# Kernel optimization log

Hardware: AMD Instinct MI355X
Metric: run time of the kernel (lower is better)

## Reference

```python
import jax, jax.numpy as jnp
import numpy as np

K_NEIGH = 20
THRES = 0.5


def setup_inputs() -> dict:
    key = jax.random.key(0)
    # pairwise distance matrix: (batch, num_points, num_points)
    x = jax.random.uniform(key, (16, 4096, 4096), dtype=jnp.float32)
    return {"x": x}


def reference(x):
    # top_k over negated distances == k smallest distances
    vals, nn_idx = jax.lax.top_k(-x, K_NEIGH)          # (B, N, k)
    n = x.shape[1]
    # self index per row, broadcast over k (matches to_add tile in TF code)
    self_idx = jnp.broadcast_to(
        jnp.arange(n, dtype=nn_idx.dtype)[:, None], (n, K_NEIGH)
    )                                                   # (N, k)
    # where distance > thres (i.e. vals < -thres), replace neighbor with self
    mask = vals < -THRES                                # (B, N, k) bool
    nn_idx = jnp.where(mask, self_idx[None, :, :], nn_idx)
    return jax.lax.stop_gradient(nn_idx)
```

## Files before the change

### kernel.cpp

```cpp
#include <hip/hip_runtime.h>
#include <stdint.h>

#define K_NEIGH 20
#define THRES   0.5f
#define NPTS    4096
#define BLOCK   256
#define CAP     256

__global__ __launch_bounds__(BLOCK)
void knn_topk_kernel(const float* __restrict__ x, int* __restrict__ out) {
    const int row  = blockIdx.x;
    const int self = row & (NPTS - 1);
    const int tid  = threadIdx.x;
    const float* __restrict__ xr = x + (size_t)row * NPTS;

    float v[16];
#pragma unroll
    for (int m = 0; m < 4; ++m) {
        float4 f = ((const float4*)xr)[tid + 256 * m];
        v[4*m+0] = f.x; v[4*m+1] = f.y; v[4*m+2] = f.z; v[4*m+3] = f.w;
    }

    __shared__ unsigned long long keys[CAP];
    __shared__ int cnt;
    __shared__ unsigned long long warpmin[4];

    if (tid == 0) cnt = 0;
    __syncthreads();

    const float T = 0.02f;
    int local = 0;
#pragma unroll
    for (int e = 0; e < 16; ++e) local += (v[e] < T) ? 1 : 0;

    int base = 0;
    if (local) base = atomicAdd(&cnt, local);
    if (local && base + local <= CAP) {
        int o = base;
#pragma unroll
        for (int m = 0; m < 4; ++m) {
#pragma unroll
            for (int j = 0; j < 4; ++j) {
                float val = v[4*m + j];
                if (val < T) {
                    unsigned idx = 4u*tid + 1024u*m + j;
                    keys[o++] = ((unsigned long long)__float_as_uint(val) << 32) | idx;
                }
            }
        }
    }
    __syncthreads();
    const int total = cnt;

    if (total >= K_NEIGH && total <= CAP) {
        if (tid >= total) keys[tid] = ~0ULL;
        __syncthreads();
        for (int k = 2; k <= CAP; k <<= 1) {
            for (int j = k >> 1; j > 0; j >>= 1) {
                int ixj = tid ^ j;
                if (ixj > tid) {
                    unsigned long long a = keys[tid];
                    unsigned long long b = keys[ixj];
                    bool up = ((tid & k) == 0);
                    if ((a > b) == up) { keys[tid] = b; keys[ixj] = a; }
                }
                __syncthreads();
            }
        }
        if (tid < K_NEIGH) {
            unsigned long long kk = keys[tid];
            float val = __uint_as_float((unsigned)(kk >> 32));
            int   idx = (int)(kk & 0xFFFFFFFFu);
            out[(size_t)row * K_NEIGH + tid] = (val > THRES) ? self : idx;
        }
    } else {
        for (int sel = 0; sel < K_NEIGH; ++sel) {
            unsigned long long best = ~0ULL;
#pragma unroll
            for (int m = 0; m < 4; ++m) {
#pragma unroll
                for (int j = 0; j < 4; ++j) {
                    unsigned long long kk =
                        ((unsigned long long)__float_as_uint(v[4*m + j]) << 32) |
                        (4u*tid + 1024u*m + j);
                    if (kk < best) best = kk;
                }
            }
            for (int off = 32; off; off >>= 1) {
                unsigned long long o = __shfl_down(best, off);
                if (o < best) best = o;
            }
            if ((tid & 63) == 0) warpmin[tid >> 6] = best;
            __syncthreads();
            if (tid == 0) {
                unsigned long long b0 = warpmin[0];
                for (int w = 1; w < 4; ++w) if (warpmin[w] < b0) b0 = warpmin[w];
                warpmin[0] = b0;
            }
            __syncthreads();
            unsigned long long win = warpmin[0];
            if (tid == 0) {
                float val = __uint_as_float((unsigned)(win >> 32));
                int   idx = (int)(win & 0xFFFFFFFFu);
                out[(size_t)row * K_NEIGH + sel] = (val > THRES) ? self : idx;
            }
            unsigned widx  = (unsigned)(win & 0xFFFFFFFFu);
            int      owner = (int)((widx >> 2) & 255u);
            if (tid == owner) v[4*(widx >> 10) + (widx & 3u)] = __uint_as_float(0x7F800000u);
            __syncthreads();
        }
    }
}

extern "C" void kernel_launch(void* const* d_in, const int* in_sizes, int n_in,
                              void* d_out, int out_size, void* d_ws, size_t ws_size,
                              hipStream_t stream) {
    const float* x  = (const float*)d_in[0];
    int*        out = (int*)d_out;
    const int n_rows = in_sizes[0] / NPTS;
    knn_topk_kernel<<<n_rows, BLOCK, 0, stream>>>(x, out);
}
```

Measured before the change: 1.427 ms.

## Process one row per wavefront and replace bitonic sort with shuffle selection

Each 64-lane wavefront now handles a whole row instead of a 256-thread block per row, so a block covers four rows and no block-level barriers are needed. The candidate keys are selected with 20 rounds of wave-wide shuffle-min over four registers per lane, replacing the shared-memory bitonic sort. The fallback path uses a strictly-increasing-key selection instead of owner invalidation. Each lane now holds 64 floats, which raises register pressure and may limit occupancy despite the launch bound hint. The shared atomic counter per wave is read without a barrier, relying on wave-synchronous execution.

```diff
diff --git a/kernel.cpp b/kernel.cpp
--- a/kernel.cpp
+++ b/kernel.cpp
@@ -4,111 +4,106 @@
 #define K_NEIGH 20
 #define THRES   0.5f
 #define NPTS    4096
-#define BLOCK   256
+#define WAVES   4
+#define BLOCK   (64 * WAVES)
 #define CAP     256
+#define TCAND   0.02f
 
-__global__ __launch_bounds__(BLOCK)
-void knn_topk_kernel(const float* __restrict__ x, int* __restrict__ out) {
-    const int row  = blockIdx.x;
+__global__ __launch_bounds__(BLOCK, 4)
+void knn_topk_wave(const float* __restrict__ x, int* __restrict__ out) {
+    const int wave = threadIdx.x >> 6;
+    const int lane = threadIdx.x & 63;
+    const int row  = blockIdx.x * WAVES + wave;
     const int self = row & (NPTS - 1);
-    const int tid  = threadIdx.x;
     const float* __restrict__ xr = x + (size_t)row * NPTS;
 
-    float v[16];
+    __shared__ unsigned long long keys[WAVES][CAP];
+    __shared__ int cnt[WAVES];
+
+    if (lane == 0) cnt[wave] = 0;
+
+    float4 f[16];
 #pragma unroll
-    for (int m = 0; m < 4; ++m) {
-        float4 f = ((const float4*)xr)[tid + 256 * m];
-        v[4*m+0] = f.x; v[4*m+1] = f.y; v[4*m+2] = f.z; v[4*m+3] = f.w;
+    for (int m = 0; m < 16; ++m) f[m] = ((const float4*)xr)[lane + 64 * m];
+
+    int local = 0;
+#pragma unroll
+    for (int m = 0; m < 16; ++m) {
+        local += (f[m].x < TCAND) + (f[m].y < TCAND) +
+                 (f[m].z < TCAND) + (f[m].w < TCAND);
     }
 
-    __shared__ unsigned long long keys[CAP];
-    __shared__ int cnt;
-    __shared__ unsigned long long warpmin[4];
-
-    if (tid == 0) cnt = 0;
-    __syncthreads();
-
-    const float T = 0.02f;
-    int local = 0;
-#pragma unroll
-    for (int e = 0; e < 16; ++e) local += (v[e] < T) ? 1 : 0;
-
     int base = 0;
-    if (local) base = atomicAdd(&cnt, local);
+    if (local) base = atomicAdd(&cnt[wave], local);
     if (local && base + local <= CAP) {
         int o = base;
 #pragma unroll
-        for (int m = 0; m < 4; ++m) {
+        for (int m = 0; m < 16; ++m) {
+            const unsigned eb = 4u * ((unsigned)lane + 64u * m);
+            const float vv[4] = { f[m].x, f[m].y, f[m].z, f[m].w };
 #pragma unroll
             for (int j = 0; j < 4; ++j) {
-                float val = v[4*m + j];
-                if (val < T) {
-                    unsigned idx = 4u*tid + 1024u*m + j;
-                    keys[o++] = ((unsigned long long)__float_as_uint(val) << 32) | idx;
+                if (vv[j] < TCAND) {
+                    keys[wave][o++] =
+                        ((unsigned long long)__float_as_uint(vv[j]) << 32) | (eb + j);
                 }
             }
         }
     }
-    __syncthreads();
-    const int total = cnt;
 
-    if (total >= K_NEIGH && total <= CAP) {
-        if (tid >= total) keys[tid] = ~0ULL;
-        __syncthreads();
-        for (int k = 2; k <= CAP; k <<= 1) {
-            for (int j = k >> 1; j > 0; j >>= 1) {
-                int ixj = tid ^ j;
-                if (ixj > tid) {
-                    unsigned long long a = keys[tid];
-                    unsigned long long b = keys[ixj];
-                    bool up = ((tid & k) == 0);
-                    if ((a > b) == up) { keys[tid] = b; keys[ixj] = a; }
-                }
-                __syncthreads();
+    const int C = cnt[wave];
+    unsigned long long mine = ~0ULL;
+
+    if (C >= K_NEIGH && C <= CAP) {
+        unsigned long long s0 = (lane       < C) ? keys[wave][lane      ] : ~0ULL;
+        unsigned long long s1 = (lane + 64  < C) ? keys[wave][lane + 64 ] : ~0ULL;
+        unsigned long long s2 = (lane + 128 < C) ? keys[wave][lane + 128] : ~0ULL;
+        unsigned long long s3 = (lane + 192 < C) ? keys[wave][lane + 192] : ~0ULL;
+#pragma unroll
+        for (int sel = 0; sel < K_NEIGH; ++sel) {
+            unsigned long long a0 = (s0 < s1) ? s0 : s1;
+            unsigned long long a1 = (s2 < s3) ? s2 : s3;
+            unsigned long long b  = (a0 < a1) ? a0 : a1;
+#pragma unroll
+            for (int off = 1; off < 64; off <<= 1) {
+                unsigned long long o = __shfl_xor(b, off);
+                b = (o < b) ? o : b;
             }
-        }
-        if (tid < K_NEIGH) {
-            unsigned long long kk = keys[tid];
-            float val = __uint_as_float((unsigned)(kk >> 32));
-            int   idx = (int)(kk & 0xFFFFFFFFu);
-            out[(size_t)row * K_NEIGH + tid] = (val > THRES) ? self : idx;
+            if (s0 == b) s0 = ~0ULL;
+            if (s1 == b) s1 = ~0ULL;
+            if (s2 == b) s2 = ~0ULL;
+            if (s3 == b) s3 = ~0ULL;
+            if (lane == sel) mine = b;
         }
     } else {
+        unsigned long long prev = 0ULL;
+        bool first = true;
         for (int sel = 0; sel < K_NEIGH; ++sel) {
-            unsigned long long best = ~0ULL;
+            unsigned long long b = ~0ULL;
 #pragma unroll
-            for (int m = 0; m < 4; ++m) {
+            for (int m = 0; m < 16; ++m) {
+                const unsigned eb = 4u * ((unsigned)lane + 64u * m);
+                const float vv[4] = { f[m].x, f[m].y, f[m].z, f[m].w };
 #pragma unroll
                 for (int j = 0; j < 4; ++j) {
                     unsigned long long kk =
-                        ((unsigned long long)__float_as_uint(v[4*m + j]) << 32) |
-                        (4u*tid + 1024u*m + j);
-                    if (kk < best) best = kk;
+                        ((unsigned long long)__float_as_uint(vv[j]) << 32) | (eb + j);
+                    if ((first || kk > prev) && kk < b) b = kk;
                 }
             }
-            for (int off = 32; off; off >>= 1) {
-                unsigned long long o = __shfl_down(best, off);
-                if (o < best) best = o;
+            for (int off = 1; off < 64; off <<= 1) {
+                unsigned long long o = __shfl_xor(b, off);
+                b = (o < b) ? o : b;
             }
-            if ((tid & 63) == 0) warpmin[tid >> 6] = best;
-            __syncthreads();
-            if (tid == 0) {
-                unsigned long long b0 = warpmin[0];
-                for (int w = 1; w < 4; ++w) if (warpmin[w] < b0) b0 = warpmin[w];
-                warpmin[0] = b0;
-            }
-            __syncthreads();
-            unsigned long long win = warpmin[0];
-            if (tid == 0) {
-                float val = __uint_as_float((unsigned)(win >> 32));
-                int   idx = (int)(win & 0xFFFFFFFFu);
-                out[(size_t)row * K_NEIGH + sel] = (val > THRES) ? self : idx;
-            }
-            unsigned widx  = (unsigned)(win & 0xFFFFFFFFu);
-            int      owner = (int)((widx >> 2) & 255u);
-            if (tid == owner) v[4*(widx >> 10) + (widx & 3u)] = __uint_as_float(0x7F800000u);
-            __syncthreads();
+            prev = b; first = false;
+            if (lane == sel) mine = b;
         }
+    }
+
+    if (lane < K_NEIGH) {
+        float val = __uint_as_float((unsigned)(mine >> 32));
+        int   idx = (int)(mine & 0xFFFFFFFFu);
+        out[(size_t)row * K_NEIGH + lane] = (val > THRES) ? self : idx;
     }
 }
 
@@ -117,6 +112,7 @@
                               hipStream_t stream) {
     const float* x  = (const float*)d_in[0];
     int*        out = (int*)d_out;
-    const int n_rows = in_sizes[0] / NPTS;
-    knn_topk_kernel<<<n_rows, BLOCK, 0, stream>>>(x, out);
+    const int n_rows  = in_sizes[0] / NPTS;
+    const int n_blocks = n_rows / WAVES;
+    knn_topk_wave<<<n_blocks, BLOCK, 0, stream>>>(x, out);
 }
```

Result: faster. 1.349 ms (-5.5%).
